# Optimization experiments

Hardware: AMD Instinct MI355X
Metric: run time of the kernel (lower is better)

Reference implementation:

```python
import jax, jax.numpy as jnp
import numpy as np

B, T, D, H, L = 8, 150, 30, 5, 3
HD = D // H  # 6
ORIG = (300, 74, 35)


def setup_inputs() -> dict:
    key = jax.random.key(0)
    ks = iter(jax.random.split(key, 40))
    def g(shape, s=0.05):
        return jax.random.normal(next(ks), shape, dtype=jnp.float32) * s
    return {
        "x_l": g((B, T, ORIG[0]), 1.0),
        "x_a": g((B, T, ORIG[1]), 1.0),
        "x_v": g((B, T, ORIG[2]), 1.0),
        "Wl": g((D, ORIG[0])),
        "Wa": g((D, ORIG[1])),
        "Wv": g((D, ORIG[2])),
        "in_w": g((2, L, 3 * D, D)),
        "in_b": jnp.zeros((2, L, 3 * D), jnp.float32),
        "out_w": g((2, L, D, D)),
        "out_b": jnp.zeros((2, L, D), jnp.float32),
        "lin1_w": g((2, L, 4 * D, D)),
        "lin1_b": jnp.zeros((2, L, 4 * D), jnp.float32),
        "lin2_w": g((2, L, D, 4 * D)),
        "lin2_b": jnp.zeros((2, L, D), jnp.float32),
        "n1_g": jnp.ones((2, L, D), jnp.float32),
        "n1_b": jnp.zeros((2, L, D), jnp.float32),
        "n2_g": jnp.ones((2, L, D), jnp.float32),
        "n2_b": jnp.zeros((2, L, D), jnp.float32),
        "p1_w": g((2 * D, 2 * D)),
        "p1_b": jnp.zeros((2 * D,), jnp.float32),
        "p2_w": g((2 * D, 2 * D)),
        "p2_b": jnp.zeros((2 * D,), jnp.float32),
        "ow": g((1, 2 * D)),
        "ob": jnp.zeros((1,), jnp.float32),
    }


def _ln(x, g, b, eps=1e-5):
    m = x.mean(-1, keepdims=True)
    v = jnp.var(x, axis=-1, keepdims=True)  # biased var, matches torch LayerNorm
    return (x - m) * jax.lax.rsqrt(v + eps) * g + b


def _heads(x):  # [Tt, B, D] -> [B*H, Tt, HD]
    Tt = x.shape[0]
    return x.reshape(Tt, B * H, HD).transpose(1, 0, 2)


def _layer(x, xk, xv, p):
    iw, ib, ow, ob, w1, b1, w2, b2, g1, bb1, g2, bb2 = p
    res = x
    xn, kn, vn = _ln(x, g1, bb1), _ln(xk, g1, bb1), _ln(xv, g1, bb1)
    q = (xn @ iw[:D].T + ib[:D]) * (HD ** -0.5)
    k = kn @ iw[D:2 * D].T + ib[D:2 * D]
    v = vn @ iw[2 * D:].T + ib[2 * D:]
    qh, kh, vh = _heads(q), _heads(k), _heads(v)
    # trilinear scores: [B*H, Tq, Tk, Tv]
    aw = jnp.einsum('iat,ibt,ict->iabc', qh, kh, vh)
    fused = aw.mean(-1) + aw.max(-1)          # fuse over value axis -> [B*H, Tq, Tk]
    fused = jax.nn.softmax(fused, axis=-1)
    attn = jnp.einsum('iab,ibt->iat', fused, qh)  # NB: original bmm uses q, not v
    attn = attn.transpose(1, 0, 2).reshape(-1, B, D)
    x = res + (attn @ ow.T + ob)
    res = x
    xn = _ln(x, g2, bb2)
    x = jax.nn.relu(xn @ w1.T + b1) @ w2.T + b2
    return res + x


def reference(x_l, x_a, x_v, Wl, Wa, Wv, in_w, in_b, out_w, out_b,
              lin1_w, lin1_b, lin2_w, lin2_b, n1_g, n1_b, n2_g, n2_b,
              p1_w, p1_b, p2_w, p2_b, ow, ob):
    pl = (x_l @ Wl.T).transpose(1, 0, 2)  # [T, B, D] (conv1d k=1, no bias)
    pa = (x_a @ Wa.T).transpose(1, 0, 2)
    pv = (x_v @ Wv.T).transpose(1, 0, 2)
    hs = []
    for s, (kk, vv) in enumerate(((pa, pv), (pv, pa))):
        h = pl
        for l in range(L):
            p = (in_w[s, l], in_b[s, l], out_w[s, l], out_b[s, l],
                 lin1_w[s, l], lin1_b[s, l], lin2_w[s, l], lin2_b[s, l],
                 n1_g[s, l], n1_b[s, l], n2_g[s, l], n2_b[s, l])
            h = _layer(h, kk, vv, p)
        hs.append(h[-1])  # last timestep [B, D]
    last_hs = jnp.concatenate(hs, axis=1)  # [B, 2D]
    proj = jax.nn.relu(last_hs @ p1_w.T + p1_b) @ p2_w.T + p2_b + last_hs
    out = proj @ ow.T + ob
    return (out, last_hs)
```

## Files before the change

kernel.cpp:

```cpp
#include <hip/hip_runtime.h>
#include <math.h>

#define BB 8
#define TT 150
#define DD 30
#define HH 5
#define HD 6
#define LL 3
#define NI 40
#define ROWF (TT*BB*DD)
#define RSTR 8
#define NR 152

typedef _Float16 half8 __attribute__((ext_vector_type(8)));
typedef float f32x16 __attribute__((ext_vector_type(16)));

__device__ __forceinline__ float wsum(float v) {
    #pragma unroll
    for (int m = 32; m > 0; m >>= 1) v += __shfl_xor(v, m, 64);
    return v;
}

__global__ __launch_bounds__(256) void proj3_kernel(
    const float* __restrict__ x_l, const float* __restrict__ x_a, const float* __restrict__ x_v,
    const float* __restrict__ Wl, const float* __restrict__ Wa, const float* __restrict__ Wv,
    float* __restrict__ pl, float* __restrict__ pa, float* __restrict__ pv) {
    int blk = blockIdx.x;
    int which = blk / 300;
    int w = threadIdx.x >> 6, lane = threadIdx.x & 63;
    int rowu = (blk % 300) * 4 + w;
    int t = rowu / BB, b = rowu % BB;
    const float* x = which == 0 ? x_l : (which == 1 ? x_a : x_v);
    const float* W = which == 0 ? Wl : (which == 1 ? Wa : Wv);
    float* out = which == 0 ? pl : (which == 1 ? pa : pv);
    int Cin = which == 0 ? 300 : (which == 1 ? 74 : 35);
    int cst = Cin + ((Cin & 1) ? 0 : 1);
    __shared__ float WS[30 * 301];
    __shared__ float xr[4][304];
    for (int j = threadIdx.x; j < DD * Cin; j += 256)
        WS[(j / Cin) * cst + (j % Cin)] = W[j];
    const float* xp = x + ((size_t)b * TT + t) * Cin;
    for (int j = lane; j < Cin; j += 64) xr[w][j] = xp[j];
    __syncthreads();
    int d = lane >> 1, jh = lane & 1;
    int h1 = Cin >> 1;
    int j0 = jh ? h1 : 0, j1 = jh ? Cin : h1;
    const float* wr = WS + (size_t)(d < DD ? d : 0) * cst;
    float acc = 0.f;
    for (int j = j0; j < j1; j++) acc += xr[w][j] * wr[j];
    acc += __shfl_xor(acc, 1, 64);
    if (jh == 0 && d < DD) out[t * (BB * DD) + b * DD + d] = acc;
}

__global__ __launch_bounds__(256) void lnqkv_kernel(
    const float* __restrict__ h, const float* __restrict__ pl,
    const float* __restrict__ pa, const float* __restrict__ pv,
    const float* __restrict__ in_w, const float* __restrict__ in_b,
    const float* __restrict__ n1g, const float* __restrict__ n1b, int l,
    float* __restrict__ q, float* __restrict__ k, float* __restrict__ v) {
    int blk = blockIdx.x;
    int s = blk / 300;
    int w = threadIdx.x >> 6, lane = threadIdx.x & 63;
    int tb = (blk % 300) * 4 + w;
    int t = tb / BB, b = tb % BB;
    const float* xk = (s == 0) ? pa : pv;
    const float* xv = (s == 0) ? pv : pa;
    int po = s * LL + l;
    const float* iw = in_w + (size_t)po * 90 * 30;
    const float* ib = in_b + (size_t)po * 90;
    const float* g  = n1g + (size_t)po * 30;
    const float* bbv = n1b + (size_t)po * 30;
    __shared__ float iwS[2700];
    __shared__ float xn[4][3][30];
    for (int j = threadIdx.x; j < 2700; j += 256) iwS[j] = iw[j];
    const float* rows[3];
    rows[0] = (l == 0) ? (pl + (size_t)tb * 30) : (h + (size_t)s * ROWF + (size_t)tb * 30);
    rows[1] = xk + (size_t)tb * 30;
    rows[2] = xv + (size_t)tb * 30;
    for (int r = 0; r < 3; r++) {
        float xval = (lane < 30) ? rows[r][lane] : 0.f;
        float mean = wsum(xval) * (1.f / 30.f);
        float dv = (lane < 30) ? (xval - mean) : 0.f;
        float var = wsum(dv * dv) * (1.f / 30.f);
        float inv = rsqrtf(var + 1e-5f);
        if (lane < 30) xn[w][r][lane] = dv * inv * g[lane] + bbv[lane];
    }
    __syncthreads();
    for (int o = lane; o < 90; o += 64) {
        int which = o / 30, dd = o % 30;
        const float* wr = iwS + o * 30;
        const float* xr = xn[w][which];
        float acc = 0.f;
        #pragma unroll 6
        for (int j = 0; j < 30; j++) acc += wr[j] * xr[j];
        acc += ib[o];
        if (which == 0) acc *= 0.40824829046386307f;
        int i = b * HH + dd / HD, hd = dd % HD;
        float* dst = (which == 0) ? q : ((which == 1) ? k : v);
        dst[((size_t)s * NI + i) * (TT * HD) + t * HD + hd] = acc;
    }
}

__global__ __launch_bounds__(256) void score_kernel(
    const float* __restrict__ q, const float* __restrict__ k, const float* __restrict__ v,
    float* __restrict__ attn) {
    int blk = blockIdx.x;
    int s = blk / 760;
    int rem = blk % 760;
    int i = rem / 19;
    int g = rem % 19;
    int tid = threadIdx.x;
    int wv = tid >> 6, lane = tid & 63;
    int lo = lane & 31, hf = lane >> 5;

    __shared__ __align__(16) _Float16 qsh[NR * RSTR];
    __shared__ __align__(16) _Float16 ksh[NR * RSTR];
    __shared__ __align__(16) _Float16 vsh[NR * RSTR];

    int* qz = (int*)qsh; int* kz = (int*)ksh; int* vz = (int*)vsh;
    for (int idx = tid; idx < NR * RSTR / 2; idx += 256) {
        qz[idx] = 0; kz[idx] = 0; vz[idx] = 0;
    }
    __syncthreads();
    const float* qg = q + (size_t)(s * NI + i) * (TT * HD);
    const float* kg = k + (size_t)(s * NI + i) * (TT * HD);
    const float* vg = v + (size_t)(s * NI + i) * (TT * HD);
    for (int idx = tid; idx < TT * HD; idx += 256) {
        int dst = (idx / HD) * RSTR + (idx % HD);
        qsh[dst] = (_Float16)qg[idx];
        ksh[dst] = (_Float16)kg[idx];
        vsh[dst] = (_Float16)vg[idx];
    }
    __syncthreads();
    if (wv == 0) {
        float v6[6] = {0.f, 0.f, 0.f, 0.f, 0.f, 0.f};
        for (int c = lane; c < TT; c += 64) {
            #pragma unroll
            for (int t = 0; t < 6; t++) v6[t] += (float)vsh[c * RSTR + t];
        }
        #pragma unroll
        for (int m = 32; m > 0; m >>= 1) {
            #pragma unroll
            for (int t = 0; t < 6; t++) v6[t] += __shfl_xor(v6[t], m, 64);
        }
        if (lane < 6) vsh[TT * RSTR + lane] = (_Float16)(v6[lane] * (1.f / TT));
    }
    __syncthreads();

    f32x16 zacc;
    #pragma unroll
    for (int j = 0; j < 16; j++) zacc[j] = 0.f;
    half8 zero8;
    #pragma unroll
    for (int t = 0; t < 8; t++) zero8[t] = (_Float16)0.f;

    half8 bfrag[5], vhalf[5];
    #pragma unroll
    for (int nt = 0; nt < 5; nt++) {
        int rr = nt * 32 + lo;
        int rc = rr < 151 ? rr : 151;
        half8 kf = *(const half8*)&ksh[rc * RSTR];
        half8 vf = *(const half8*)&vsh[rc * RSTR];
        bfrag[nt] = hf ? zero8 : kf;
        vhalf[nt] = hf ? zero8 : vf;
    }

    for (int ap = 0; ap < 2; ap++) {
        int a = g * 8 + wv * 2 + ap;
        if (a >= TT) break;
        half8 qav = *(const half8*)&qsh[a * RSTR];
        half8 afrag[5];
        #pragma unroll
        for (int nt = 0; nt < 5; nt++) afrag[nt] = vhalf[nt] * qav;

        float fsc[5];
        #pragma unroll
        for (int nb = 0; nb < 5; nb++) {
            float rm = -INFINITY;
            #pragma unroll
            for (int ma = 0; ma < 4; ma++) {
                f32x16 acc = __builtin_amdgcn_mfma_f32_32x32x16_f16(afrag[ma], bfrag[nb], zacc, 0, 0, 0);
                float m = fmaxf(acc[0], acc[1]);
                #pragma unroll
                for (int j = 2; j < 16; j += 2) m = fmaxf(fmaxf(m, acc[j]), acc[j + 1]);
                rm = fmaxf(rm, m);
            }
            f32x16 a4 = __builtin_amdgcn_mfma_f32_32x32x16_f16(afrag[4], bfrag[nb], zacc, 0, 0, 0);
            float m4 = fmaxf(a4[0], a4[1]);
            #pragma unroll
            for (int j = 2; j < 10; j += 2) m4 = fmaxf(fmaxf(m4, a4[j]), a4[j + 1]);
            float ext = (hf == 0) ? fmaxf(a4[10], a4[11]) : -INFINITY;
            rm = fmaxf(rm, fmaxf(m4, ext));
            float om = __shfl_xor(a4[10], 32, 64);
            float mn = hf ? a4[10] : om;
            rm = fmaxf(rm, __shfl_xor(rm, 32, 64));
            int bcol = nb * 32 + lo;
            fsc[nb] = (bcol < TT) ? (mn + rm) : -INFINITY;
        }
        float m = fsc[0];
        #pragma unroll
        for (int nb = 1; nb < 5; nb++) m = fmaxf(m, fsc[nb]);
        #pragma unroll
        for (int msk = 16; msk > 0; msk >>= 1) m = fmaxf(m, __shfl_xor(m, msk, 64));
        float e[5], es = 0.f;
        #pragma unroll
        for (int nb = 0; nb < 5; nb++) { e[nb] = __expf(fsc[nb] - m); es += e[nb]; }
        #pragma unroll
        for (int msk = 16; msk > 0; msk >>= 1) es += __shfl_xor(es, msk, 64);
        float acc6[6] = {0.f, 0.f, 0.f, 0.f, 0.f, 0.f};
        #pragma unroll
        for (int nb = 0; nb < 5; nb++) {
            int bcol = nb * 32 + lo;
            int bi = (bcol < TT) ? bcol : 0;
            float wgt = e[nb];
            half8 qrow = *(const half8*)&qsh[bi * RSTR];
            #pragma unroll
            for (int t = 0; t < 6; t++) acc6[t] += wgt * (float)qrow[t];
        }
        #pragma unroll
        for (int msk = 16; msk > 0; msk >>= 1) {
            #pragma unroll
            for (int t = 0; t < 6; t++) acc6[t] += __shfl_xor(acc6[t], msk, 64);
        }
        if (lane == 0) {
            float inv = 1.f / es;
            int bo = i / HH, ho = i % HH;
            float* dst = attn + (size_t)s * ROWF + a * (BB * DD) + bo * DD + ho * HD;
            #pragma unroll
            for (int t = 0; t < 6; t++) dst[t] = acc6[t] * inv;
        }
    }
}

__global__ __launch_bounds__(256) void ffn_kernel(
    const float* __restrict__ attn, const float* __restrict__ pl,
    const float* __restrict__ out_w, const float* __restrict__ out_b,
    const float* __restrict__ l1w, const float* __restrict__ l1b,
    const float* __restrict__ l2w, const float* __restrict__ l2b,
    const float* __restrict__ n2g, const float* __restrict__ n2b, int l,
    float* __restrict__ h) {
    int blk = blockIdx.x;
    int s = blk / 300;
    int w = threadIdx.x >> 6, lane = threadIdx.x & 63;
    int tb = (blk % 300) * 4 + w;
    int po = s * LL + l;
    const float* ow = out_w + (size_t)po * 900;
    const float* ob = out_b + (size_t)po * 30;
    const float* w1 = l1w + (size_t)po * 120 * 30;
    const float* b1 = l1b + (size_t)po * 120;
    const float* w2 = l2w + (size_t)po * 30 * 120;
    const float* b2 = l2b + (size_t)po * 30;
    const float* g  = n2g + (size_t)po * 30;
    const float* bbv = n2b + (size_t)po * 30;
    __shared__ float owS[900];
    __shared__ float w1S[3600];
    __shared__ float w2S[30 * 121];
    __shared__ float arS[4][30], xnS[4][32], hidS[4][120];
    for (int j = threadIdx.x; j < 900; j += 256) owS[j] = ow[j];
    for (int j = threadIdx.x; j < 3600; j += 256) w1S[j] = w1[j];
    for (int j = threadIdx.x; j < 3600; j += 256) w2S[(j / 120) * 121 + (j % 120)] = w2[j];
    __syncthreads();
    float* hrow = h + (size_t)s * ROWF + (size_t)tb * 30;
    const float* res = (l == 0) ? (pl + (size_t)tb * 30) : hrow;
    const float* arow = attn + (size_t)s * ROWF + (size_t)tb * 30;
    if (lane < 30) arS[w][lane] = arow[lane];
    float x1v = 0.f;
    if (lane < 30) {
        const float* wr = owS + lane * 30;
        float acc = 0.f;
        #pragma unroll 6
        for (int j = 0; j < 30; j++) acc += wr[j] * arS[w][j];
        x1v = res[lane] + acc + ob[lane];
    }
    float mean = wsum(x1v) * (1.f / 30.f);
    float dv = (lane < 30) ? (x1v - mean) : 0.f;
    float var = wsum(dv * dv) * (1.f / 30.f);
    float inv = rsqrtf(var + 1e-5f);
    if (lane < 30) xnS[w][lane] = dv * inv * g[lane] + bbv[lane];
    for (int o = lane; o < 120; o += 64) {
        const float* wr = w1S + o * 30;
        float acc = 0.f;
        #pragma unroll 6
        for (int j = 0; j < 30; j++) acc += wr[j] * xnS[w][j];
        hidS[w][o] = fmaxf(acc + b1[o], 0.f);
    }
    if (lane < 30) {
        const float* wr = w2S + lane * 121;
        float acc = 0.f;
        #pragma unroll 8
        for (int j = 0; j < 120; j++) acc += wr[j] * hidS[w][j];
        hrow[lane] = x1v + acc + b2[lane];
    }
}

__global__ __launch_bounds__(256) void head_kernel(
    const float* __restrict__ h,
    const float* __restrict__ p1w, const float* __restrict__ p1b,
    const float* __restrict__ p2w, const float* __restrict__ p2b,
    const float* __restrict__ ow, const float* __restrict__ ob,
    float* __restrict__ out) {
    int tid = threadIdx.x;
    __shared__ float lh[480], hid[480], pr[480];
    for (int idx = tid; idx < 480; idx += 256) {
        int b = idx / 60, j = idx % 60;
        int s = j / 30, d = j % 30;
        float vv = h[(size_t)s * ROWF + 149 * (BB * DD) + b * DD + d];
        lh[idx] = vv;
        out[8 + idx] = vv;
    }
    __syncthreads();
    for (int idx = tid; idx < 480; idx += 256) {
        int b = idx / 60, o = idx % 60;
        const float* wr = p1w + o * 60;
        float acc = p1b[o];
        for (int j = 0; j < 60; j++) acc += wr[j] * lh[b * 60 + j];
        hid[idx] = fmaxf(acc, 0.f);
    }
    __syncthreads();
    for (int idx = tid; idx < 480; idx += 256) {
        int b = idx / 60, d = idx % 60;
        const float* wr = p2w + d * 60;
        float acc = p2b[d];
        for (int j = 0; j < 60; j++) acc += wr[j] * hid[b * 60 + j];
        pr[idx] = acc + lh[idx];
    }
    __syncthreads();
    if (tid < 8) {
        float acc = ob[0];
        for (int j = 0; j < 60; j++) acc += pr[tid * 60 + j] * ow[j];
        out[tid] = acc;
    }
}

extern "C" void kernel_launch(void* const* d_in, const int* in_sizes, int n_in,
                              void* d_out, int out_size, void* d_ws, size_t ws_size,
                              hipStream_t stream) {
    const float* x_l   = (const float*)d_in[0];
    const float* x_a   = (const float*)d_in[1];
    const float* x_v   = (const float*)d_in[2];
    const float* Wl    = (const float*)d_in[3];
    const float* Wa    = (const float*)d_in[4];
    const float* Wv    = (const float*)d_in[5];
    const float* in_w  = (const float*)d_in[6];
    const float* in_b  = (const float*)d_in[7];
    const float* out_w = (const float*)d_in[8];
    const float* out_b = (const float*)d_in[9];
    const float* l1w   = (const float*)d_in[10];
    const float* l1b   = (const float*)d_in[11];
    const float* l2w   = (const float*)d_in[12];
    const float* l2b   = (const float*)d_in[13];
    const float* n1g   = (const float*)d_in[14];
    const float* n1b   = (const float*)d_in[15];
    const float* n2g   = (const float*)d_in[16];
    const float* n2b   = (const float*)d_in[17];
    const float* p1w   = (const float*)d_in[18];
    const float* p1b   = (const float*)d_in[19];
    const float* p2w   = (const float*)d_in[20];
    const float* p2b   = (const float*)d_in[21];
    const float* oww   = (const float*)d_in[22];
    const float* obb   = (const float*)d_in[23];

    float* ws = (float*)d_ws;
    float* pl = ws;
    float* pa = ws + 36000;
    float* pv = ws + 72000;
    float* h  = ws + 108000;
    float* q  = ws + 180000;
    float* kk = ws + 252000;
    float* vv = ws + 324000;
    float* at = ws + 396000;

    proj3_kernel<<<900, 256, 0, stream>>>(x_l, x_a, x_v, Wl, Wa, Wv, pl, pa, pv);

    for (int l = 0; l < LL; l++) {
        lnqkv_kernel<<<600, 256, 0, stream>>>(h, pl, pa, pv, in_w, in_b, n1g, n1b, l, q, kk, vv);
        score_kernel<<<1520, 256, 0, stream>>>(q, kk, vv, at);
        ffn_kernel<<<600, 256, 0, stream>>>(at, pl, out_w, out_b, l1w, l1b, l2w, l2b,
                                            n2g, n2b, l, h);
    }
    head_kernel<<<1, 256, 0, stream>>>(h, p1w, p1b, p2w, p2b, oww, obb, (float*)d_out);
}
```

Measured before the change: 261.4 us.

## Precompute K/V for all layers and fuse next-layer Q projection into FFN

K and V depend only on the fixed pa/pv inputs, so all six (stream, layer) K/V projections are now computed up front in one kernel. The next layer's LayerNorm and Q projection are folded into the tail of the FFN kernel, and a separate kernel computes Q for layer 0. Per layer this cuts the launch count from three to two and avoids re-reading h for the Q projection. The w1 shared-memory layout is also transposed to avoid bank conflicts. In exchange the workspace grows and the FFN kernel uses more shared memory.

```diff
diff --git a/kernel.cpp b/kernel.cpp
--- a/kernel.cpp
+++ b/kernel.cpp
@@ -52,58 +52,92 @@
     if (jh == 0 && d < DD) out[t * (BB * DD) + b * DD + d] = acc;
 }
 
-__global__ __launch_bounds__(256) void lnqkv_kernel(
-    const float* __restrict__ h, const float* __restrict__ pl,
+__global__ __launch_bounds__(256) void kvpre_kernel(
     const float* __restrict__ pa, const float* __restrict__ pv,
     const float* __restrict__ in_w, const float* __restrict__ in_b,
-    const float* __restrict__ n1g, const float* __restrict__ n1b, int l,
-    float* __restrict__ q, float* __restrict__ k, float* __restrict__ v) {
+    const float* __restrict__ n1g, const float* __restrict__ n1b,
+    float* __restrict__ k_all, float* __restrict__ v_all) {
     int blk = blockIdx.x;
-    int s = blk / 300;
+    int po = blk / 300;
+    int s = po / LL;
     int w = threadIdx.x >> 6, lane = threadIdx.x & 63;
     int tb = (blk % 300) * 4 + w;
     int t = tb / BB, b = tb % BB;
     const float* xk = (s == 0) ? pa : pv;
     const float* xv = (s == 0) ? pv : pa;
-    int po = s * LL + l;
-    const float* iw = in_w + (size_t)po * 90 * 30;
+    const float* iw = in_w + (size_t)po * 2700 + 900;
     const float* ib = in_b + (size_t)po * 90;
     const float* g  = n1g + (size_t)po * 30;
-    const float* bbv = n1b + (size_t)po * 30;
-    __shared__ float iwS[2700];
-    __shared__ float xn[4][3][30];
-    for (int j = threadIdx.x; j < 2700; j += 256) iwS[j] = iw[j];
-    const float* rows[3];
-    rows[0] = (l == 0) ? (pl + (size_t)tb * 30) : (h + (size_t)s * ROWF + (size_t)tb * 30);
-    rows[1] = xk + (size_t)tb * 30;
-    rows[2] = xv + (size_t)tb * 30;
-    for (int r = 0; r < 3; r++) {
+    const float* bb = n1b + (size_t)po * 30;
+    __shared__ float iwS[1800];
+    __shared__ float xn[4][2][30];
+    for (int j = threadIdx.x; j < 1800; j += 256) iwS[j] = iw[j];
+    const float* rows[2] = { xk + (size_t)tb * 30, xv + (size_t)tb * 30 };
+    for (int r = 0; r < 2; r++) {
         float xval = (lane < 30) ? rows[r][lane] : 0.f;
         float mean = wsum(xval) * (1.f / 30.f);
         float dv = (lane < 30) ? (xval - mean) : 0.f;
         float var = wsum(dv * dv) * (1.f / 30.f);
         float inv = rsqrtf(var + 1e-5f);
-        if (lane < 30) xn[w][r][lane] = dv * inv * g[lane] + bbv[lane];
-    }
-    __syncthreads();
-    for (int o = lane; o < 90; o += 64) {
+        if (lane < 30) xn[w][r][lane] = dv * inv * g[lane] + bb[lane];
+    }
+    __syncthreads();
+    int o = lane;
+    if (o < 60) {
         int which = o / 30, dd = o % 30;
         const float* wr = iwS + o * 30;
         const float* xr = xn[w][which];
         float acc = 0.f;
         #pragma unroll 6
         for (int j = 0; j < 30; j++) acc += wr[j] * xr[j];
-        acc += ib[o];
-        if (which == 0) acc *= 0.40824829046386307f;
+        acc += ib[30 + o];
         int i = b * HH + dd / HD, hd = dd % HD;
-        float* dst = (which == 0) ? q : ((which == 1) ? k : v);
-        dst[((size_t)s * NI + i) * (TT * HD) + t * HD + hd] = acc;
+        float* dst = which ? v_all : k_all;
+        dst[((size_t)po * NI + i) * (TT * HD) + t * HD + hd] = acc;
+    }
+}
+
+__global__ __launch_bounds__(256) void lnq0_kernel(
+    const float* __restrict__ pl,
+    const float* __restrict__ in_w, const float* __restrict__ in_b,
+    const float* __restrict__ n1g, const float* __restrict__ n1b,
+    float* __restrict__ q) {
+    int blk = blockIdx.x;
+    int s = blk / 300;
+    int w = threadIdx.x >> 6, lane = threadIdx.x & 63;
+    int tb = (blk % 300) * 4 + w;
+    int t = tb / BB, b = tb % BB;
+    int po = s * LL;
+    const float* iw = in_w + (size_t)po * 2700;
+    const float* ib = in_b + (size_t)po * 90;
+    const float* g  = n1g + (size_t)po * 30;
+    const float* bb = n1b + (size_t)po * 30;
+    __shared__ float iwS[900];
+    __shared__ float xn[4][30];
+    for (int j = threadIdx.x; j < 900; j += 256) iwS[j] = iw[j];
+    const float* row = pl + (size_t)tb * 30;
+    float xval = (lane < 30) ? row[lane] : 0.f;
+    float mean = wsum(xval) * (1.f / 30.f);
+    float dv = (lane < 30) ? (xval - mean) : 0.f;
+    float var = wsum(dv * dv) * (1.f / 30.f);
+    float inv = rsqrtf(var + 1e-5f);
+    if (lane < 30) xn[w][lane] = dv * inv * g[lane] + bb[lane];
+    __syncthreads();
+    int o = lane;
+    if (o < 30) {
+        const float* wr = iwS + o * 30;
+        float acc = 0.f;
+        #pragma unroll 6
+        for (int j = 0; j < 30; j++) acc += wr[j] * xn[w][j];
+        acc = (acc + ib[o]) * 0.40824829046386307f;
+        int i = b * HH + o / HD, hd = o % HD;
+        q[((size_t)s * NI + i) * (TT * HD) + t * HD + hd] = acc;
     }
 }
 
 __global__ __launch_bounds__(256) void score_kernel(
-    const float* __restrict__ q, const float* __restrict__ k, const float* __restrict__ v,
-    float* __restrict__ attn) {
+    const float* __restrict__ q, const float* __restrict__ k_all,
+    const float* __restrict__ v_all, int l, float* __restrict__ attn) {
     int blk = blockIdx.x;
     int s = blk / 760;
     int rem = blk % 760;
@@ -112,6 +146,7 @@
     int tid = threadIdx.x;
     int wv = tid >> 6, lane = tid & 63;
     int lo = lane & 31, hf = lane >> 5;
+    int po = s * LL + l;
 
     __shared__ __align__(16) _Float16 qsh[NR * RSTR];
     __shared__ __align__(16) _Float16 ksh[NR * RSTR];
@@ -123,8 +158,8 @@
     }
     __syncthreads();
     const float* qg = q + (size_t)(s * NI + i) * (TT * HD);
-    const float* kg = k + (size_t)(s * NI + i) * (TT * HD);
-    const float* vg = v + (size_t)(s * NI + i) * (TT * HD);
+    const float* kg = k_all + (size_t)(po * NI + i) * (TT * HD);
+    const float* vg = v_all + (size_t)(po * NI + i) * (TT * HD);
     for (int idx = tid; idx < TT * HD; idx += 256) {
         int dst = (idx / HD) * RSTR + (idx % HD);
         qsh[dst] = (_Float16)qg[idx];
@@ -232,33 +267,42 @@
     }
 }
 
-__global__ __launch_bounds__(256) void ffn_kernel(
+__global__ __launch_bounds__(256) void ffnlnq_kernel(
     const float* __restrict__ attn, const float* __restrict__ pl,
     const float* __restrict__ out_w, const float* __restrict__ out_b,
     const float* __restrict__ l1w, const float* __restrict__ l1b,
     const float* __restrict__ l2w, const float* __restrict__ l2b,
-    const float* __restrict__ n2g, const float* __restrict__ n2b, int l,
-    float* __restrict__ h) {
+    const float* __restrict__ n2g, const float* __restrict__ n2b,
+    const float* __restrict__ in_w, const float* __restrict__ in_b,
+    const float* __restrict__ n1g, const float* __restrict__ n1b,
+    int l, int has_next,
+    float* __restrict__ h, float* __restrict__ q) {
     int blk = blockIdx.x;
     int s = blk / 300;
     int w = threadIdx.x >> 6, lane = threadIdx.x & 63;
     int tb = (blk % 300) * 4 + w;
+    int t = tb / BB, b = tb % BB;
     int po = s * LL + l;
     const float* ow = out_w + (size_t)po * 900;
     const float* ob = out_b + (size_t)po * 30;
-    const float* w1 = l1w + (size_t)po * 120 * 30;
+    const float* w1 = l1w + (size_t)po * 3600;
     const float* b1 = l1b + (size_t)po * 120;
-    const float* w2 = l2w + (size_t)po * 30 * 120;
+    const float* w2 = l2w + (size_t)po * 3600;
     const float* b2 = l2b + (size_t)po * 30;
-    const float* g  = n2g + (size_t)po * 30;
-    const float* bbv = n2b + (size_t)po * 30;
+    const float* g2 = n2g + (size_t)po * 30;
+    const float* bb2 = n2b + (size_t)po * 30;
     __shared__ float owS[900];
-    __shared__ float w1S[3600];
+    __shared__ float w1T[30 * 128];
     __shared__ float w2S[30 * 121];
-    __shared__ float arS[4][30], xnS[4][32], hidS[4][120];
+    __shared__ float iwqS[900];
+    __shared__ float arS[4][30], xnS[4][32], hidS[4][120], xqS[4][30];
     for (int j = threadIdx.x; j < 900; j += 256) owS[j] = ow[j];
-    for (int j = threadIdx.x; j < 3600; j += 256) w1S[j] = w1[j];
+    for (int j = threadIdx.x; j < 3600; j += 256) w1T[(j % 30) * 128 + (j / 30)] = w1[j];
     for (int j = threadIdx.x; j < 3600; j += 256) w2S[(j / 120) * 121 + (j % 120)] = w2[j];
+    if (has_next) {
+        const float* iwq = in_w + (size_t)(po + 1) * 2700;
+        for (int j = threadIdx.x; j < 900; j += 256) iwqS[j] = iwq[j];
+    }
     __syncthreads();
     float* hrow = h + (size_t)s * ROWF + (size_t)tb * 30;
     const float* res = (l == 0) ? (pl + (size_t)tb * 30) : hrow;
@@ -276,20 +320,41 @@
     float dv = (lane < 30) ? (x1v - mean) : 0.f;
     float var = wsum(dv * dv) * (1.f / 30.f);
     float inv = rsqrtf(var + 1e-5f);
-    if (lane < 30) xnS[w][lane] = dv * inv * g[lane] + bbv[lane];
+    if (lane < 30) xnS[w][lane] = dv * inv * g2[lane] + bb2[lane];
     for (int o = lane; o < 120; o += 64) {
-        const float* wr = w1S + o * 30;
         float acc = 0.f;
         #pragma unroll 6
-        for (int j = 0; j < 30; j++) acc += wr[j] * xnS[w][j];
+        for (int j = 0; j < 30; j++) acc += w1T[j * 128 + o] * xnS[w][j];
         hidS[w][o] = fmaxf(acc + b1[o], 0.f);
     }
+    float newh = 0.f;
     if (lane < 30) {
         const float* wr = w2S + lane * 121;
         float acc = 0.f;
         #pragma unroll 8
         for (int j = 0; j < 120; j++) acc += wr[j] * hidS[w][j];
-        hrow[lane] = x1v + acc + b2[lane];
+        newh = x1v + acc + b2[lane];
+        hrow[lane] = newh;
+    }
+    if (has_next) {
+        const float* g1 = n1g + (size_t)(po + 1) * 30;
+        const float* bb1 = n1b + (size_t)(po + 1) * 30;
+        const float* ibq = in_b + (size_t)(po + 1) * 90;
+        float mean2 = wsum(newh) * (1.f / 30.f);
+        float dv2 = (lane < 30) ? (newh - mean2) : 0.f;
+        float var2 = wsum(dv2 * dv2) * (1.f / 30.f);
+        float inv2 = rsqrtf(var2 + 1e-5f);
+        if (lane < 30) xqS[w][lane] = dv2 * inv2 * g1[lane] + bb1[lane];
+        int o = lane;
+        if (o < 30) {
+            const float* wr = iwqS + o * 30;
+            float acc = 0.f;
+            #pragma unroll 6
+            for (int j = 0; j < 30; j++) acc += wr[j] * xqS[w][j];
+            acc = (acc + ibq[o]) * 0.40824829046386307f;
+            int i = b * HH + o / HD, hd = o % HD;
+            q[((size_t)s * NI + i) * (TT * HD) + t * HD + hd] = acc;
+        }
     }
 }
 
@@ -361,22 +426,24 @@
     const float* obb   = (const float*)d_in[23];
 
     float* ws = (float*)d_ws;
-    float* pl = ws;
-    float* pa = ws + 36000;
-    float* pv = ws + 72000;
-    float* h  = ws + 108000;
-    float* q  = ws + 180000;
-    float* kk = ws + 252000;
-    float* vv = ws + 324000;
-    float* at = ws + 396000;
+    float* pl    = ws;
+    float* pa    = ws + 36000;
+    float* pv    = ws + 72000;
+    float* h     = ws + 108000;
+    float* q     = ws + 180000;
+    float* k_all = ws + 252000;
+    float* v_all = ws + 468000;
+    float* at    = ws + 684000;
 
     proj3_kernel<<<900, 256, 0, stream>>>(x_l, x_a, x_v, Wl, Wa, Wv, pl, pa, pv);
+    kvpre_kernel<<<1800, 256, 0, stream>>>(pa, pv, in_w, in_b, n1g, n1b, k_all, v_all);
+    lnq0_kernel<<<600, 256, 0, stream>>>(pl, in_w, in_b, n1g, n1b, q);
 
     for (int l = 0; l < LL; l++) {
-        lnqkv_kernel<<<600, 256, 0, stream>>>(h, pl, pa, pv, in_w, in_b, n1g, n1b, l, q, kk, vv);
-        score_kernel<<<1520, 256, 0, stream>>>(q, kk, vv, at);
-        ffn_kernel<<<600, 256, 0, stream>>>(at, pl, out_w, out_b, l1w, l1b, l2w, l2b,
-                                            n2g, n2b, l, h);
+        score_kernel<<<1520, 256, 0, stream>>>(q, k_all, v_all, l, at);
+        ffnlnq_kernel<<<600, 256, 0, stream>>>(at, pl, out_w, out_b, l1w, l1b, l2w, l2b,
+                                               n2g, n2b, in_w, in_b, n1g, n1b,
+                                               l, (l < LL - 1) ? 1 : 0, h, q);
     }
     head_kernel<<<1, 256, 0, stream>>>(h, p1w, p1b, p2w, p2b, oww, obb, (float*)d_out);
 }
```

After: 254.2 us. 2.8% less time.
